# Performance work log

Measured on AMD Instinct MI355X. Metric: run time of the kernel, lower is better.

Reference implementation:

```python
import jax, jax.numpy as jnp
import numpy as np

B, C, H, W = 8, 384, 32, 32
HEADS = 12


def _relative_position_index(h, w):
    coords_h = np.arange(h)
    coords_w = np.arange(w)
    coords = np.stack(np.meshgrid(coords_h, coords_w, indexing='ij'))  # [2,h,w]
    flat = coords.reshape(2, -1)  # [2, N]
    rel = flat[:, :, None] - flat[:, None, :]  # [2, N, N]
    rel = rel.transpose(1, 2, 0)  # [N, N, 2]
    rel[:, :, 0] += h - 1
    rel[:, :, 1] += w - 1
    rel[:, :, 0] *= 2 * w - 1
    return rel.sum(-1).astype(np.int32)  # [N, N]


def setup_inputs() -> dict:
    key = jax.random.key(0)
    ks = jax.random.split(key, 6)
    std = 0.02
    x = jax.random.normal(ks[0], (B, C, H, W), dtype=jnp.float32)
    q_w = jax.random.normal(ks[1], (C, C), dtype=jnp.float32) * std
    q_b = jnp.zeros((C,), dtype=jnp.float32)
    kv_w = jax.random.normal(ks[2], (2 * C, C), dtype=jnp.float32) * std
    kv_b = jnp.zeros((2 * C,), dtype=jnp.float32)
    proj_w = jax.random.normal(ks[3], (C, C), dtype=jnp.float32) * std
    proj_b = jnp.zeros((C,), dtype=jnp.float32)
    n_table = (2 * H - 1) * (2 * W - 1)
    rpb_table = jax.random.normal(ks[4], (n_table, HEADS), dtype=jnp.float32) * std
    rel_index = jnp.asarray(_relative_position_index(H, W))  # [N, N] int32
    return {"x": x, "q_w": q_w, "q_b": q_b, "kv_w": kv_w, "kv_b": kv_b,
            "proj_w": proj_w, "proj_b": proj_b, "rpb_table": rpb_table,
            "rel_index": rel_index}


def reference(x, q_w, q_b, kv_w, kv_b, proj_w, proj_b, rpb_table, rel_index):
    b, c, h, w = x.shape
    n = h * w
    heads = rpb_table.shape[-1]
    hd = c // heads
    scale = hd ** (-0.5)

    xf = x.reshape(b, c, n)  # 1x1 conv == per-pixel matmul
    q = jnp.einsum('dc,bcn->bdn', q_w, xf) + q_b[:, None]
    q = q.reshape(b, heads, hd, n).transpose(0, 1, 3, 2)  # [b,h,n,hd]
    kv = jnp.einsum('dc,bcn->bdn', kv_w, xf) + kv_b[:, None]
    kv = kv.reshape(b, 2, heads, hd, n)
    k = kv[:, 0].transpose(0, 1, 3, 2)  # [b,h,n,hd]
    v = kv[:, 1].transpose(0, 1, 3, 2)

    attn = jnp.einsum('bhnd,bhmd->bhnm', q, k) * scale  # [b,h,n,n]
    bias = rpb_table[rel_index.reshape(-1)].reshape(n, n, heads)
    bias = bias.transpose(2, 0, 1)  # [h,n,n]
    attn = jax.nn.softmax(attn + bias[None], axis=-1)

    out = jnp.einsum('bhnm,bhmd->bhnd', attn, v)
    out = out.transpose(0, 1, 3, 2).reshape(b, c, h, w)
    out = jnp.einsum('dc,bchw->bdhw', proj_w, out) + proj_b[None, :, None, None]
    return out
```

## Files before the change

kernel.cpp:

```cpp
#include <hip/hip_runtime.h>
#include <hip/hip_bf16.h>

#define B_  8
#define C_  384
#define N_  1024
#define NH_ 12
#define HD_ 32
#define D3_ 1152

typedef __bf16 bf16x8 __attribute__((ext_vector_type(8)));
typedef __bf16 bf16x2 __attribute__((ext_vector_type(2)));
typedef float  f32x4  __attribute__((ext_vector_type(4)));

typedef const __attribute__((address_space(1))) unsigned int guint;
typedef __attribute__((address_space(3))) unsigned int luint;

__device__ __forceinline__ float b2f(ushort u) {
    return __uint_as_float(((unsigned int)u) << 16);
}
__device__ __forceinline__ ushort f2b(float f) {
    unsigned int i = __float_as_uint(f);
    unsigned int r = i + 0x7fffu + ((i >> 16) & 1u);
    return (ushort)(r >> 16);
}
__device__ __forceinline__ unsigned pk2(float a, float b) {
#if __has_builtin(__builtin_amdgcn_cvt_pk_bf16_f32)
    bf16x2 t = __builtin_amdgcn_cvt_pk_bf16_f32(a, b);
    return __builtin_bit_cast(unsigned, t);
#else
    return (unsigned)f2b(a) | ((unsigned)f2b(b) << 16);
#endif
}

#if __has_builtin(__builtin_amdgcn_exp2f)
#define EXP2 __builtin_amdgcn_exp2f
#else
#define EXP2 exp2f
#endif

__device__ __forceinline__ void gl2lds16(const void* g, void* l) {
    __builtin_amdgcn_global_load_lds((guint*)g, (luint*)l, 16, 0, 0);
}

#define C1_ 0.25505654204433796f
#define C2_ 1.4426950408889634f
#define TS_ 3972

__global__ __launch_bounds__(256) void setup(
    const float* __restrict__ x, const float* __restrict__ q_w,
    const float* __restrict__ kv_w, const float* __restrict__ proj_w,
    const float* __restrict__ q_b, const float* __restrict__ kv_b,
    const float* __restrict__ tab,
    ushort* __restrict__ xT, float* __restrict__ tabT,
    ushort* __restrict__ Wall, ushort* __restrict__ PW,
    float* __restrict__ ballf)
{
    __shared__ ushort T[64 * 72];
    const int bx = blockIdx.x, tid = threadIdx.x;

    if (bx < 768) {
        int t = bx;
        int nx = t & 15, cy = (t >> 4) % 6, b = t / 96;
        int n0 = nx * 64, c0 = cy * 64;
        {
            int i = tid >> 2;
            int ns = (tid & 3) * 16;
            const float* src = x + ((size_t)b * C_ + c0 + i) * N_ + n0 + ns;
            #pragma unroll
            for (int k4 = 0; k4 < 4; ++k4) {
                float4 f = *(const float4*)(src + k4 * 4);
                T[(ns + k4 * 4 + 0) * 72 + i] = f2b(f.x);
                T[(ns + k4 * 4 + 1) * 72 + i] = f2b(f.y);
                T[(ns + k4 * 4 + 2) * 72 + i] = f2b(f.z);
                T[(ns + k4 * 4 + 3) * 72 + i] = f2b(f.w);
            }
        }
        __syncthreads();
        {
            int j = tid >> 2;
            int cs = (tid & 3) * 16;
            ushort* dst = xT + ((size_t)b * N_ + n0 + j) * C_ + c0 + cs;
            *(uint4*)dst       = *(const uint4*)&T[j * 72 + cs];
            *(uint4*)(dst + 8) = *(const uint4*)&T[j * 72 + cs + 8];
        }
    } else if (bx < 1346) {
        const int NW4 = 110592, NP4 = 36864, NB4 = 288;
        int t = (bx - 768) * 256 + tid;
        if (t < NW4) {
            int e = t * 4;
            float4 f = (e < 147456) ? *(const float4*)(q_w + e)
                                    : *(const float4*)(kv_w + e - 147456);
            union { uint2 u; ushort s[4]; } o;
            o.u.x = pk2(f.x, f.y); o.u.y = pk2(f.z, f.w);
            *(uint2*)(Wall + e) = o.u;
        } else if (t < NW4 + NP4) {
            int e = (t - NW4) * 4;
            float4 f = *(const float4*)(proj_w + e);
            union { uint2 u; ushort s[4]; } o;
            o.u.x = pk2(f.x, f.y); o.u.y = pk2(f.z, f.w);
            *(uint2*)(PW + e) = o.u;
        } else if (t < NW4 + NP4 + NB4) {
            int e = (t - NW4 - NP4) * 4;
            float4 f = (e < 384) ? *(const float4*)(q_b + e)
                                 : *(const float4*)(kv_b + e - 384);
            *(float4*)(ballf + e) = f;
        }
    } else {
        int h = bx - 1346;
        for (int i = tid; i < 3969; i += 256)
            tabT[h * TS_ + i] = tab[(size_t)(3968 - i) * NH_ + h] * C2_;
        if (tid < 3) tabT[h * TS_ + 3969 + tid] = 0.0f;
    }
}

__global__ __launch_bounds__(256) void qkv_gemm5(
    const ushort* __restrict__ xT, const ushort* __restrict__ Wall,
    const float* __restrict__ ballf, ushort* __restrict__ Qt,
    ushort* __restrict__ Kt, ushort* __restrict__ Vtc)
{
    const int b = blockIdx.z, n0 = blockIdx.x * 128, d0 = blockIdx.y * 128;
    __shared__ ushort As[128 * 32];
    __shared__ ushort Bs[128 * 32];
    const int tid = threadIdx.x;
    const int lane = tid & 63, wave = tid >> 6;
    const int quad = lane >> 4, l16 = lane & 15;
    const int wn = (wave & 1) * 64, wd = (wave >> 1) * 64;

    f32x4 acc[4][4] = {};
    const ushort* xb = xT + ((size_t)b * N_ + n0) * C_;
    const ushort* wb = Wall + (size_t)d0 * C_;
    const int rowA = wave * 16 + (lane >> 2);
    const int fstage = ((lane >> 2) ^ (lane >> 4)) & 3;
    const int coff = ((lane & 3) ^ fstage) * 8;
    const int fread = ((l16 & 3) ^ ((l16 >> 2) & 3));
    const bool isV = (d0 >= 768);

    for (int c0 = 0; c0 < C_; c0 += 32) {
        #pragma unroll
        for (int k = 0; k < 2; ++k) {
            gl2lds16(xb + (size_t)(k * 64 + rowA) * C_ + c0 + coff,
                     &As[(size_t)(k * 256 + wave * 64) * 8]);
            gl2lds16(wb + (size_t)(k * 64 + rowA) * C_ + c0 + coff,
                     &Bs[(size_t)(k * 256 + wave * 64) * 8]);
        }
        __syncthreads();
        bf16x8 af[4], bfr[4];
        #pragma unroll
        for (int i = 0; i < 4; ++i)
            af[i] = *(const bf16x8*)&As[(wn + i * 16 + l16) * 32 + (quad ^ fread) * 8];
        #pragma unroll
        for (int j = 0; j < 4; ++j)
            bfr[j] = *(const bf16x8*)&Bs[(wd + j * 16 + l16) * 32 + (quad ^ fread) * 8];
        if (!isV) {
            #pragma unroll
            for (int i = 0; i < 4; ++i)
                #pragma unroll
                for (int j = 0; j < 4; ++j)
                    acc[i][j] = __builtin_amdgcn_mfma_f32_16x16x32_bf16(bfr[i], af[j], acc[i][j], 0, 0, 0);
        } else {
            #pragma unroll
            for (int i = 0; i < 4; ++i)
                #pragma unroll
                for (int j = 0; j < 4; ++j)
                    acc[i][j] = __builtin_amdgcn_mfma_f32_16x16x32_bf16(af[i], bfr[j], acc[i][j], 0, 0, 0);
        }
        __syncthreads();
    }

    if (!isV) {
        ushort* dst = (d0 < 384) ? Qt : Kt;
        const float sc = (d0 < 384) ? C1_ : 1.0f;
        const int reg0 = (d0 < 384) ? 0 : 384;
        #pragma unroll
        for (int i = 0; i < 4; ++i) {
            int dloc = wd + i * 16;
            int dg = d0 - reg0 + dloc;
            int h = dg >> 5;
            int dc = (dg & 31) + quad * 4;
            float4 bvv = *(const float4*)(ballf + d0 + dloc + quad * 4);
            size_t hb = (size_t)(b * NH_ + h) * N_;
            #pragma unroll
            for (int j = 0; j < 4; ++j) {
                int n = n0 + wn + j * 16 + l16;
                uint2 w;
                w.x = pk2((acc[i][j][0] + bvv.x) * sc, (acc[i][j][1] + bvv.y) * sc);
                w.y = pk2((acc[i][j][2] + bvv.z) * sc, (acc[i][j][3] + bvv.w) * sc);
                *(uint2*)(dst + (hb + n) * 32 + dc) = w;
            }
        }
    } else {
        #pragma unroll
        for (int j = 0; j < 4; ++j) {
            int dloc = wd + j * 16 + l16;
            int vd = d0 - 768 + dloc;
            int h = vd >> 5, dc = vd & 31;
            float bv = ballf[d0 + dloc];
            size_t hbase = (size_t)(b * NH_ + h) * 32768 + dc * 32;
            #pragma unroll
            for (int i = 0; i < 4; ++i) {
                int n = n0 + wn + i * 16 + quad * 4;
                size_t cbase = hbase + (size_t)((n >> 5)) * 1024 + (n & 31);
                uint2 w;
                w.x = pk2(acc[i][j][0] + bv, acc[i][j][1] + bv);
                w.y = pk2(acc[i][j][2] + bv, acc[i][j][3] + bv);
                *(uint2*)(Vtc + cbase) = w;
            }
        }
    }
}

__global__ __launch_bounds__(256) void attn5(
    const ushort* __restrict__ Qt, const ushort* __restrict__ Kt,
    const ushort* __restrict__ Vtc, const float* __restrict__ tabT,
    ushort* __restrict__ O)
{
    const int bid = blockIdx.x;
    const int bh96 = bid % 96;
    const int nx = bid / 96;
    const int b = bh96 / 12, h = bh96 % 12;

    __shared__ float tabL[TS_];
    __shared__ ushort Pa[8192];

    const int tid = threadIdx.x;
    const int lane = tid & 63, wave = tid >> 6;
    const int quad = lane >> 4, l16 = lane & 15;
    const int bh = b * NH_ + h;

    {
        const float* th = tabT + h * TS_;
        int i = tid * 4;
        #pragma unroll
        for (int k = 0; k < 4; ++k) {
            if (i < TS_) *(float4*)&tabL[i] = *(const float4*)&th[i];
            i += 1024;
        }
    }
    __syncthreads();

    const int qs0 = nx * 8 + wave * 2;
    const ushort* Kbh = Kt + (size_t)bh * N_ * 32;
    const ushort* Vbh = Vtc + (size_t)bh * 16 * 2048;

    bf16x8 qf[2];
    #pragma unroll
    for (int st = 0; st < 2; ++st) {
        int q = (qs0 + st) * 16 + l16;
        qf[st] = *(const bf16x8*)(Qt + ((size_t)bh * N_ + q) * 32 + quad * 8);
    }
    int ibx0;
    {
        int q = qs0 * 16 + l16;
        ibx0 = (31 - (q >> 5)) * 63 + (31 - (q & 31));
    }

    f32x4 oacc[2][2] = {};
    float rs[2] = {0.f, 0.f};

    ushort* PwBase = &Pa[wave * 2048];
    const int pswz = l16 & 0xE;

    for (int mc = 0; mc < 16; ++mc) {
        const ushort* kp = Kbh + mc * 64 * 32;
        bf16x8 k0 = *(const bf16x8*)(kp + (0 * 16 + l16) * 32 + quad * 8);
        bf16x8 k1 = *(const bf16x8*)(kp + (1 * 16 + l16) * 32 + quad * 8);
        bf16x8 k2 = *(const bf16x8*)(kp + (2 * 16 + l16) * 32 + quad * 8);
        bf16x8 k3 = *(const bf16x8*)(kp + (3 * 16 + l16) * 32 + quad * 8);
        const ushort* vp = Vbh + mc * 2048;
        bf16x8 va[2][2];
        #pragma unroll
        for (int kc = 0; kc < 2; ++kc)
            #pragma unroll
            for (int dt = 0; dt < 2; ++dt)
                va[kc][dt] = *(const bf16x8*)(vp + kc * 1024 + (dt * 16 + l16) * 32 + quad * 8);

        const float* Tb = tabL + ibx0 + mc * 126 + quad * 4;
        f32x4 tvm16, tv0, tv16, tv47, tv63, tv79;
        #pragma unroll
        for (int e = 0; e < 4; ++e) {
            tvm16[e] = Tb[e - 16];
            tv0[e]   = Tb[e];
            tv16[e]  = Tb[e + 16];
            tv47[e]  = Tb[e + 47];
            tv63[e]  = Tb[e + 63];
            tv79[e]  = Tb[e + 79];
        }
        f32x4 cbs[2][4] = {{tv0, tv16, tv63, tv79}, {tvm16, tv0, tv47, tv63}};

        #pragma unroll
        for (int st = 0; st < 2; ++st) {
            f32x4 s0 = __builtin_amdgcn_mfma_f32_16x16x32_bf16(k0, qf[st], cbs[st][0], 0, 0, 0);
            f32x4 s1 = __builtin_amdgcn_mfma_f32_16x16x32_bf16(k1, qf[st], cbs[st][1], 0, 0, 0);
            f32x4 s2 = __builtin_amdgcn_mfma_f32_16x16x32_bf16(k2, qf[st], cbs[st][2], 0, 0, 0);
            f32x4 s3 = __builtin_amdgcn_mfma_f32_16x16x32_bf16(k3, qf[st], cbs[st][3], 0, 0, 0);

            ushort* Pw = PwBase + st * 1024;
            f32x4 sv[4] = {s0, s1, s2, s3};
            #pragma unroll
            for (int t = 0; t < 4; ++t) {
                float p0 = EXP2(sv[t][0]);
                float p1 = EXP2(sv[t][1]);
                float p2 = EXP2(sv[t][2]);
                float p3 = EXP2(sv[t][3]);
                rs[st] += (p0 + p1) + (p2 + p3);
                uint2 w;
                w.x = pk2(p0, p1);
                w.y = pk2(p2, p3);
                *(uint2*)(Pw + l16 * 64 + (((t * 4 + quad) ^ pswz) * 4)) = w;
            }
            #pragma unroll
            for (int kc = 0; kc < 2; ++kc) {
                bf16x8 pb = *(const bf16x8*)(Pw + l16 * 64 + (((kc * 8 + quad * 2) ^ pswz) * 4));
                oacc[st][0] = __builtin_amdgcn_mfma_f32_16x16x32_bf16(va[kc][0], pb, oacc[st][0], 0, 0, 0);
                oacc[st][1] = __builtin_amdgcn_mfma_f32_16x16x32_bf16(va[kc][1], pb, oacc[st][1], 0, 0, 0);
            }
        }
    }

    #pragma unroll
    for (int st = 0; st < 2; ++st) {
        float s = rs[st];
        s += __shfl_xor(s, 16, 64);
        s += __shfl_xor(s, 32, 64);
        rs[st] = 1.0f / s;
    }

    #pragma unroll
    for (int st = 0; st < 2; ++st) {
        int q = (qs0 + st) * 16 + l16;
        ushort* ob = O + ((size_t)(b * N_ + q)) * C_ + h * HD_;
        #pragma unroll
        for (int dt = 0; dt < 2; ++dt) {
            uint2 w;
            w.x = pk2(oacc[st][dt][0] * rs[st], oacc[st][dt][1] * rs[st]);
            w.y = pk2(oacc[st][dt][2] * rs[st], oacc[st][dt][3] * rs[st]);
            *(uint2*)(ob + dt * 16 + quad * 4) = w;
        }
    }
}

__global__ __launch_bounds__(256) void proj_gemm3(
    const ushort* __restrict__ O, const ushort* __restrict__ PW,
    const float* __restrict__ pb, float* __restrict__ out)
{
    const int b = blockIdx.z, n0 = blockIdx.x * 128, d0 = blockIdx.y * 128;
    __shared__ ushort As[128 * 32];
    __shared__ ushort Bs[128 * 32];
    const int tid = threadIdx.x;
    const int lane = tid & 63, wave = tid >> 6;
    const int quad = lane >> 4, l16 = lane & 15;
    const int wa = (wave & 1) * 64, wb = (wave >> 1) * 64;

    f32x4 acc[4][4] = {};
    const ushort* ab = PW + (size_t)d0 * C_;
    const ushort* bbp = O + ((size_t)b * N_ + n0) * C_;
    const int rowA = wave * 16 + (lane >> 2);
    const int fstage = ((lane >> 2) ^ (lane >> 4)) & 3;
    const int coff = ((lane & 3) ^ fstage) * 8;
    const int fread = ((l16 & 3) ^ ((l16 >> 2) & 3));

    for (int c0 = 0; c0 < C_; c0 += 32) {
        #pragma unroll
        for (int k = 0; k < 2; ++k) {
            gl2lds16(ab + (size_t)(k * 64 + rowA) * C_ + c0 + coff,
                     &As[(size_t)(k * 256 + wave * 64) * 8]);
            gl2lds16(bbp + (size_t)(k * 64 + rowA) * C_ + c0 + coff,
                     &Bs[(size_t)(k * 256 + wave * 64) * 8]);
        }
        __syncthreads();
        bf16x8 af[4], bfr[4];
        #pragma unroll
        for (int i = 0; i < 4; ++i)
            af[i] = *(const bf16x8*)&As[(wa + i * 16 + l16) * 32 + (quad ^ fread) * 8];
        #pragma unroll
        for (int j = 0; j < 4; ++j)
            bfr[j] = *(const bf16x8*)&Bs[(wb + j * 16 + l16) * 32 + (quad ^ fread) * 8];
        #pragma unroll
        for (int i = 0; i < 4; ++i)
            #pragma unroll
            for (int j = 0; j < 4; ++j)
                acc[i][j] = __builtin_amdgcn_mfma_f32_16x16x32_bf16(af[i], bfr[j], acc[i][j], 0, 0, 0);
        __syncthreads();
    }

    #pragma unroll
    for (int i = 0; i < 4; ++i) {
        #pragma unroll
        for (int r = 0; r < 4; ++r) {
            int d = d0 + wa + i * 16 + quad * 4 + r;
            float bv = pb[d];
            float* op = out + ((size_t)b * C_ + d) * N_ + n0 + wb;
            #pragma unroll
            for (int j = 0; j < 4; ++j)
                op[j * 16 + l16] = acc[i][j][r] + bv;
        }
    }
}

extern "C" void kernel_launch(void* const* d_in, const int* in_sizes, int n_in,
                              void* d_out, int out_size, void* d_ws, size_t ws_size,
                              hipStream_t stream)
{
    const float* x      = (const float*)d_in[0];
    const float* q_w    = (const float*)d_in[1];
    const float* q_b    = (const float*)d_in[2];
    const float* kv_w   = (const float*)d_in[3];
    const float* kv_b   = (const float*)d_in[4];
    const float* proj_w = (const float*)d_in[5];
    const float* proj_b = (const float*)d_in[6];
    const float* rpb    = (const float*)d_in[7];
    float* out = (float*)d_out;

    char* ws = (char*)d_ws;
    ushort* xT    = (ushort*)(ws);
    ushort* Qt    = (ushort*)(ws +  6291456);
    ushort* Kt    = (ushort*)(ws + 12582912);
    ushort* Vtc   = (ushort*)(ws + 18874368);
    ushort* O     = (ushort*)(ws + 25165824);
    float*  tabT  = (float*) (ws + 31457280);
    ushort* Wall  = (ushort*)(ws + 31647936);
    ushort* PW    = (ushort*)(ws + 32532672);
    float*  ballf = (float*) (ws + 32827584);

    setup      <<<dim3(1358), 256, 0, stream>>>(x, q_w, kv_w, proj_w, q_b, kv_b, rpb,
                                                xT, tabT, Wall, PW, ballf);
    qkv_gemm5  <<<dim3(8, 9, B_), 256, 0, stream>>>(xT, Wall, ballf, Qt, Kt, Vtc);
    attn5      <<<dim3(768), 256, 0, stream>>>(Qt, Kt, Vtc, tabT, O);
    proj_gemm3 <<<dim3(8, 3, B_), 256, 0, stream>>>(O, PW, proj_b, out);
}
```

Measured before the change: 150.9 us.

## Split attention to one query tile per wave, prefetch K, MFMA row sums

The attention kernel now gives each wave a single 16-query tile instead of two, so the grid doubles to 1536 blocks, LDS for P is halved, and launch bounds request 4 blocks per CU. The next K chunk is loaded one iteration ahead to hide global latency. The softmax row sum moves from scalar adds plus cross-lane shuffles to an extra MFMA against a ones vector. The trade-off is that K/V loads are no longer shared across two query tiles per wave, so per-query global traffic goes up and more MFMAs are issued.

```diff
diff --git a/kernel.cpp b/kernel.cpp
--- a/kernel.cpp
+++ b/kernel.cpp
@@ -209,7 +209,7 @@
     }
 }
 
-__global__ __launch_bounds__(256) void attn5(
+__global__ __launch_bounds__(256, 4) void attn6(
     const ushort* __restrict__ Qt, const ushort* __restrict__ Kt,
     const ushort* __restrict__ Vtc, const float* __restrict__ tabT,
     ushort* __restrict__ O)
@@ -220,7 +220,7 @@
     const int b = bh96 / 12, h = bh96 % 12;
 
     __shared__ float tabL[TS_];
-    __shared__ ushort Pa[8192];
+    __shared__ ushort Pa[4096];
 
     const int tid = threadIdx.x;
     const int lane = tid & 63, wave = tid >> 6;
@@ -238,105 +238,94 @@
     }
     __syncthreads();
 
-    const int qs0 = nx * 8 + wave * 2;
+    const int qs = nx * 4 + wave;
+    const int q = qs * 16 + l16;
     const ushort* Kbh = Kt + (size_t)bh * N_ * 32;
     const ushort* Vbh = Vtc + (size_t)bh * 16 * 2048;
 
-    bf16x8 qf[2];
+    bf16x8 qf = *(const bf16x8*)(Qt + ((size_t)bh * N_ + q) * 32 + quad * 8);
+    const int ibx = (31 - (q >> 5)) * 63 + (31 - (q & 31));
+
+    bf16x8 ones;
     #pragma unroll
-    for (int st = 0; st < 2; ++st) {
-        int q = (qs0 + st) * 16 + l16;
-        qf[st] = *(const bf16x8*)(Qt + ((size_t)bh * N_ + q) * 32 + quad * 8);
-    }
-    int ibx0;
-    {
-        int q = qs0 * 16 + l16;
-        ibx0 = (31 - (q >> 5)) * 63 + (31 - (q & 31));
-    }
-
-    f32x4 oacc[2][2] = {};
-    float rs[2] = {0.f, 0.f};
-
-    ushort* PwBase = &Pa[wave * 2048];
+    for (int j = 0; j < 8; ++j) ones[j] = (__bf16)1.0f;
+
+    f32x4 oacc0 = {}, oacc1 = {}, lacc = {};
+
+    ushort* Pw = &Pa[wave * 1024];
     const int pswz = l16 & 0xE;
+    const int pwr = l16 * 64;
+
+    const ushort* kp0 = Kbh + l16 * 32 + quad * 8;
+    bf16x8 ka0 = *(const bf16x8*)(kp0);
+    bf16x8 ka1 = *(const bf16x8*)(kp0 + 512);
+    bf16x8 ka2 = *(const bf16x8*)(kp0 + 1024);
+    bf16x8 ka3 = *(const bf16x8*)(kp0 + 1536);
 
     for (int mc = 0; mc < 16; ++mc) {
-        const ushort* kp = Kbh + mc * 64 * 32;
-        bf16x8 k0 = *(const bf16x8*)(kp + (0 * 16 + l16) * 32 + quad * 8);
-        bf16x8 k1 = *(const bf16x8*)(kp + (1 * 16 + l16) * 32 + quad * 8);
-        bf16x8 k2 = *(const bf16x8*)(kp + (2 * 16 + l16) * 32 + quad * 8);
-        bf16x8 k3 = *(const bf16x8*)(kp + (3 * 16 + l16) * 32 + quad * 8);
-        const ushort* vp = Vbh + mc * 2048;
-        bf16x8 va[2][2];
-        #pragma unroll
-        for (int kc = 0; kc < 2; ++kc)
-            #pragma unroll
-            for (int dt = 0; dt < 2; ++dt)
-                va[kc][dt] = *(const bf16x8*)(vp + kc * 1024 + (dt * 16 + l16) * 32 + quad * 8);
-
-        const float* Tb = tabL + ibx0 + mc * 126 + quad * 4;
-        f32x4 tvm16, tv0, tv16, tv47, tv63, tv79;
+        const ushort* vp = Vbh + mc * 2048 + l16 * 32 + quad * 8;
+        bf16x8 va00 = *(const bf16x8*)(vp);
+        bf16x8 va01 = *(const bf16x8*)(vp + 512);
+        bf16x8 va10 = *(const bf16x8*)(vp + 1024);
+        bf16x8 va11 = *(const bf16x8*)(vp + 1536);
+        const ushort* kn = Kbh + ((mc + 1) & 15) * 2048 + l16 * 32 + quad * 8;
+        bf16x8 kb0 = *(const bf16x8*)(kn);
+        bf16x8 kb1 = *(const bf16x8*)(kn + 512);
+        bf16x8 kb2 = *(const bf16x8*)(kn + 1024);
+        bf16x8 kb3 = *(const bf16x8*)(kn + 1536);
+
+        const float* Tb = tabL + ibx + mc * 126 + quad * 4;
+        f32x4 cb0, cb1, cb2, cb3;
         #pragma unroll
         for (int e = 0; e < 4; ++e) {
-            tvm16[e] = Tb[e - 16];
-            tv0[e]   = Tb[e];
-            tv16[e]  = Tb[e + 16];
-            tv47[e]  = Tb[e + 47];
-            tv63[e]  = Tb[e + 63];
-            tv79[e]  = Tb[e + 79];
-        }
-        f32x4 cbs[2][4] = {{tv0, tv16, tv63, tv79}, {tvm16, tv0, tv47, tv63}};
-
-        #pragma unroll
-        for (int st = 0; st < 2; ++st) {
-            f32x4 s0 = __builtin_amdgcn_mfma_f32_16x16x32_bf16(k0, qf[st], cbs[st][0], 0, 0, 0);
-            f32x4 s1 = __builtin_amdgcn_mfma_f32_16x16x32_bf16(k1, qf[st], cbs[st][1], 0, 0, 0);
-            f32x4 s2 = __builtin_amdgcn_mfma_f32_16x16x32_bf16(k2, qf[st], cbs[st][2], 0, 0, 0);
-            f32x4 s3 = __builtin_amdgcn_mfma_f32_16x16x32_bf16(k3, qf[st], cbs[st][3], 0, 0, 0);
-
-            ushort* Pw = PwBase + st * 1024;
-            f32x4 sv[4] = {s0, s1, s2, s3};
-            #pragma unroll
-            for (int t = 0; t < 4; ++t) {
-                float p0 = EXP2(sv[t][0]);
-                float p1 = EXP2(sv[t][1]);
-                float p2 = EXP2(sv[t][2]);
-                float p3 = EXP2(sv[t][3]);
-                rs[st] += (p0 + p1) + (p2 + p3);
-                uint2 w;
-                w.x = pk2(p0, p1);
-                w.y = pk2(p2, p3);
-                *(uint2*)(Pw + l16 * 64 + (((t * 4 + quad) ^ pswz) * 4)) = w;
-            }
-            #pragma unroll
-            for (int kc = 0; kc < 2; ++kc) {
-                bf16x8 pb = *(const bf16x8*)(Pw + l16 * 64 + (((kc * 8 + quad * 2) ^ pswz) * 4));
-                oacc[st][0] = __builtin_amdgcn_mfma_f32_16x16x32_bf16(va[kc][0], pb, oacc[st][0], 0, 0, 0);
-                oacc[st][1] = __builtin_amdgcn_mfma_f32_16x16x32_bf16(va[kc][1], pb, oacc[st][1], 0, 0, 0);
-            }
-        }
-    }
-
-    #pragma unroll
-    for (int st = 0; st < 2; ++st) {
-        float s = rs[st];
-        s += __shfl_xor(s, 16, 64);
-        s += __shfl_xor(s, 32, 64);
-        rs[st] = 1.0f / s;
-    }
-
-    #pragma unroll
-    for (int st = 0; st < 2; ++st) {
-        int q = (qs0 + st) * 16 + l16;
-        ushort* ob = O + ((size_t)(b * N_ + q)) * C_ + h * HD_;
-        #pragma unroll
-        for (int dt = 0; dt < 2; ++dt) {
+            cb0[e] = Tb[e];
+            cb1[e] = Tb[e + 16];
+            cb2[e] = Tb[e + 63];
+            cb3[e] = Tb[e + 79];
+        }
+
+        f32x4 s0 = __builtin_amdgcn_mfma_f32_16x16x32_bf16(ka0, qf, cb0, 0, 0, 0);
+        f32x4 s1 = __builtin_amdgcn_mfma_f32_16x16x32_bf16(ka1, qf, cb1, 0, 0, 0);
+        f32x4 s2 = __builtin_amdgcn_mfma_f32_16x16x32_bf16(ka2, qf, cb2, 0, 0, 0);
+        f32x4 s3 = __builtin_amdgcn_mfma_f32_16x16x32_bf16(ka3, qf, cb3, 0, 0, 0);
+        ka0 = kb0; ka1 = kb1; ka2 = kb2; ka3 = kb3;
+
+        {
             uint2 w;
-            w.x = pk2(oacc[st][dt][0] * rs[st], oacc[st][dt][1] * rs[st]);
-            w.y = pk2(oacc[st][dt][2] * rs[st], oacc[st][dt][3] * rs[st]);
-            *(uint2*)(ob + dt * 16 + quad * 4) = w;
-        }
-    }
+            w.x = pk2(EXP2(s0[0]), EXP2(s0[1]));
+            w.y = pk2(EXP2(s0[2]), EXP2(s0[3]));
+            *(uint2*)(Pw + pwr + (((0 + quad) ^ pswz) * 4)) = w;
+            w.x = pk2(EXP2(s1[0]), EXP2(s1[1]));
+            w.y = pk2(EXP2(s1[2]), EXP2(s1[3]));
+            *(uint2*)(Pw + pwr + (((4 + quad) ^ pswz) * 4)) = w;
+            w.x = pk2(EXP2(s2[0]), EXP2(s2[1]));
+            w.y = pk2(EXP2(s2[2]), EXP2(s2[3]));
+            *(uint2*)(Pw + pwr + (((8 + quad) ^ pswz) * 4)) = w;
+            w.x = pk2(EXP2(s3[0]), EXP2(s3[1]));
+            w.y = pk2(EXP2(s3[2]), EXP2(s3[3]));
+            *(uint2*)(Pw + pwr + (((12 + quad) ^ pswz) * 4)) = w;
+        }
+
+        bf16x8 pb0 = *(const bf16x8*)(Pw + pwr + (((quad * 2) ^ pswz) * 4));
+        lacc  = __builtin_amdgcn_mfma_f32_16x16x32_bf16(ones, pb0, lacc, 0, 0, 0);
+        oacc0 = __builtin_amdgcn_mfma_f32_16x16x32_bf16(va00, pb0, oacc0, 0, 0, 0);
+        oacc1 = __builtin_amdgcn_mfma_f32_16x16x32_bf16(va01, pb0, oacc1, 0, 0, 0);
+        bf16x8 pb1 = *(const bf16x8*)(Pw + pwr + (((8 + quad * 2) ^ pswz) * 4));
+        lacc  = __builtin_amdgcn_mfma_f32_16x16x32_bf16(ones, pb1, lacc, 0, 0, 0);
+        oacc0 = __builtin_amdgcn_mfma_f32_16x16x32_bf16(va10, pb1, oacc0, 0, 0, 0);
+        oacc1 = __builtin_amdgcn_mfma_f32_16x16x32_bf16(va11, pb1, oacc1, 0, 0, 0);
+    }
+
+    float inv = 1.0f / lacc[0];
+
+    ushort* ob = O + ((size_t)(b * N_ + q)) * C_ + h * HD_;
+    uint2 w0, w1;
+    w0.x = pk2(oacc0[0] * inv, oacc0[1] * inv);
+    w0.y = pk2(oacc0[2] * inv, oacc0[3] * inv);
+    *(uint2*)(ob + quad * 4) = w0;
+    w1.x = pk2(oacc1[0] * inv, oacc1[1] * inv);
+    w1.y = pk2(oacc1[2] * inv, oacc1[3] * inv);
+    *(uint2*)(ob + 16 + quad * 4) = w1;
 }
 
 __global__ __launch_bounds__(256) void proj_gemm3(
@@ -425,6 +414,6 @@
     setup      <<<dim3(1358), 256, 0, stream>>>(x, q_w, kv_w, proj_w, q_b, kv_b, rpb,
                                                 xT, tabT, Wall, PW, ballf);
     qkv_gemm5  <<<dim3(8, 9, B_), 256, 0, stream>>>(xT, Wall, ballf, Qt, Kt, Vtc);
-    attn5      <<<dim3(768), 256, 0, stream>>>(Qt, Kt, Vtc, tabT, O);
+    attn6      <<<dim3(1536), 256, 0, stream>>>(Qt, Kt, Vtc, tabT, O);
     proj_gemm3 <<<dim3(8, 3, B_), 256, 0, stream>>>(O, PW, proj_b, out);
 }
```

After: 168.9 us. 12.0% more time.
